# Kernel optimization log

Measured on AMD Instinct MI355X. Metric: run time of the kernel, lower is better.

The kernel has to match this reference:

```python
import jax, jax.numpy as jnp
import numpy as np

B, N_IN, N_OUT = 8192, 2048, 2048


def setup_inputs() -> dict:
    key = jax.random.key(0)
    kx, kw = jax.random.split(key)
    x = jax.random.normal(kx, (B, N_IN), dtype=jnp.float32)
    # torch: uniform_(-0.5, 0.5)
    weight = jax.random.uniform(kw, (N_IN, N_OUT), dtype=jnp.float32, minval=-0.5, maxval=0.5)
    return {"x": x, "weight": weight}


def reference(x, weight):
    # Binarize: W > 0 -> {0, 1}; then dense matmul (batch, n_in) @ (n_in, n_out)
    w_bin = (weight > 0).astype(x.dtype)
    return x @ w_bin
```

## Files before the change

kernel.cpp:

```cpp
#include <hip/hip_runtime.h>


#define MDIM 8192
#define NDIM 2048
#define KDIM 2048
#define NT   (KDIM / 128)
#define CH   (64 * KDIM)
#define BUFS 49152

typedef __attribute__((ext_vector_type(8))) short short8;
typedef __attribute__((ext_vector_type(4))) float float4v;
typedef __attribute__((ext_vector_type(4))) float f32x4;
typedef __attribute__((ext_vector_type(4))) int int4v;
typedef __attribute__((ext_vector_type(4))) unsigned short ushort4v;
typedef __attribute__((ext_vector_type(8))) unsigned short ushort8v;

__device__ __forceinline__ unsigned short f2bf(float f) {
    union { float f; unsigned u; } v; v.f = f;
    unsigned r = v.u + 0x7FFFu + ((v.u >> 16) & 1u);
    return (unsigned short)(r >> 16);
}

__device__ __forceinline__ void gload_lds16(void* l, const void* g) {
    __builtin_amdgcn_global_load_lds(
        (const __attribute__((address_space(1))) unsigned int*)g,
        (__attribute__((address_space(3))) unsigned int*)l,
        16, 0, 0);
}

#define FENCE asm volatile("" ::: "memory")
#define BAR do { FENCE; __builtin_amdgcn_s_barrier(); FENCE; } while (0)

__global__ __launch_bounds__(256) void prep(const float* __restrict__ X,
                                            const float* __restrict__ W,
                                            signed char* __restrict__ Xq,
                                            signed char* __restrict__ Wt,
                                            float* __restrict__ Sc) {
    __shared__ __align__(16) signed char T[64][80];
    __shared__ float wm[4];
    const int t = threadIdx.x;
    const int bid = blockIdx.x;

    if (bid < MDIM) {
        const int row = bid;
        const float* xr = X + (size_t)row * KDIM + t * 8;
        float4v a = *reinterpret_cast<const float4v*>(xr);
        float4v b = *reinterpret_cast<const float4v*>(xr + 4);
        float m = fabsf(a[0]);
        m = fmaxf(m, fabsf(a[1])); m = fmaxf(m, fabsf(a[2])); m = fmaxf(m, fabsf(a[3]));
        m = fmaxf(m, fabsf(b[0])); m = fmaxf(m, fabsf(b[1]));
        m = fmaxf(m, fabsf(b[2])); m = fmaxf(m, fabsf(b[3]));
#pragma unroll
        for (int off = 32; off; off >>= 1)
            m = fmaxf(m, __shfl_xor(m, off));
        if ((t & 63) == 0) wm[t >> 6] = m;
        __syncthreads();
        const float s = fmaxf(fmaxf(wm[0], wm[1]), fmaxf(wm[2], wm[3]));
        const float inv = (s > 0.f) ? 127.0f / s : 0.f;

        int q[8];
        q[0] = __float2int_rn(a[0] * inv); q[1] = __float2int_rn(a[1] * inv);
        q[2] = __float2int_rn(a[2] * inv); q[3] = __float2int_rn(a[3] * inv);
        q[4] = __float2int_rn(b[0] * inv); q[5] = __float2int_rn(b[1] * inv);
        q[6] = __float2int_rn(b[2] * inv); q[7] = __float2int_rn(b[3] * inv);
        unsigned lo = (q[0] & 255) | ((q[1] & 255) << 8) | ((q[2] & 255) << 16) | ((unsigned)(q[3] & 255) << 24);
        unsigned hi = (q[4] & 255) | ((q[5] & 255) << 8) | ((q[6] & 255) << 16) | ((unsigned)(q[7] & 255) << 24);
        unsigned* dst = (unsigned*)(Xq + (size_t)row * KDIM + t * 8);
        dst[0] = lo; dst[1] = hi;
        if (t == 0) Sc[row] = s * (1.0f / 127.0f);
    } else {
        const int wb = bid - MDIM;
        const int k0 = (wb >> 5) * 64;
        const int n0 = (wb & 31) * 64;
        const int kr = t >> 4;
        const int nc = (t & 15) * 4;
#pragma unroll
        for (int rr = 0; rr < 4; ++rr) {
            int k = k0 + rr * 16 + kr;
            float4v w4 = *reinterpret_cast<const float4v*>(W + (size_t)k * NDIM + n0 + nc);
#pragma unroll
            for (int c = 0; c < 4; ++c)
                T[nc + c][rr * 16 + kr] = (w4[c] > 0.0f) ? (signed char)1 : (signed char)0;
        }
        __syncthreads();
        const int row = t >> 2, ch = t & 3;
        int4v v = *reinterpret_cast<const int4v*>(&T[row][ch * 16]);
        *reinterpret_cast<int4v*>(Wt + (size_t)(n0 + row) * KDIM + k0 + ch * 16) = v;
    }
}

__global__ __launch_bounds__(512, 1) void gemm_2t(const signed char* __restrict__ A,
                                                  const signed char* __restrict__ Bt,
                                                  const float* __restrict__ Sc,
                                                  float* __restrict__ O) {
    extern __shared__ char lds[];
    const int tid  = threadIdx.x;
    const int lane = tid & 63;
    const int w    = tid >> 6;
    const int wr   = w >> 1;
    const int wc   = w & 1;

    int id  = blockIdx.x;
    int swz = (id & 7) * 32 + (id >> 3);
    const int bm  = swz >> 3;
    const int bnh = swz & 7;

    const int l3 = lane >> 3, l7 = lane & 7;
    const int srcOff = (w * 8 + l3) * KDIM + ((l7 ^ l3) << 4);
    const char* gA = (const char*)A + (size_t)(bm * 256) * KDIM + srcOff;

    const int fr = lane & 15, fg = lane >> 4;
    const int se0 = ((fg)     ^ (fr & 7)) << 4;
    const int se1 = ((4 + fg) ^ (fr & 7)) << 4;
    const int aRd = (wr * 64 + fr) * 128;
    const int bRd = 32768 + (wc * 64 + fr) * 128;

    {
        const char* gB0 = (const char*)Bt + (size_t)(bnh * 256) * KDIM + srcOff;
#pragma unroll
        for (int c = 0; c < 4; ++c)
            gload_lds16(lds + c * 8192 + w * 1024, gA + (size_t)c * CH);
#pragma unroll
        for (int c = 0; c < 2; ++c)
            gload_lds16(lds + 32768 + c * 8192 + w * 1024, gB0 + (size_t)c * CH);
    }

    for (int tt = 0; tt < 2; ++tt) {
        const char* gB  = (const char*)Bt + (size_t)(bnh * 256 + tt * 128) * KDIM + srcOff;
        const char* gB2 = (const char*)Bt + (size_t)(bnh * 256 + 128) * KDIM + srcOff;

        int4v acc[4][4];
#pragma unroll
        for (int i = 0; i < 4; ++i)
#pragma unroll
            for (int j = 0; j < 4; ++j) {
                acc[i][j][0] = 0; acc[i][j][1] = 0; acc[i][j][2] = 0; acc[i][j][3] = 0;
            }

        for (int t = 0; t < NT; ++t) {
            const int cur = (t & 1) * BUFS;
            const int nxt = ((t + 1) & 1) * BUFS;

            if (t == 0 && tt == 1) asm volatile("s_waitcnt vmcnt(63)" ::: "memory");
            else                   asm volatile("s_waitcnt vmcnt(0)" ::: "memory");
            BAR;

            if (t + 1 < NT) {
                const char* aN = gA + (size_t)(t + 1) * 128;
                const char* bN = gB + (size_t)(t + 1) * 128;
#pragma unroll
                for (int c = 0; c < 4; ++c)
                    gload_lds16(lds + nxt + c * 8192 + w * 1024, aN + (size_t)c * CH);
#pragma unroll
                for (int c = 0; c < 2; ++c)
                    gload_lds16(lds + nxt + 32768 + c * 8192 + w * 1024, bN + (size_t)c * CH);
            } else if (tt == 0) {
#pragma unroll
                for (int c = 0; c < 4; ++c)
                    gload_lds16(lds + nxt + c * 8192 + w * 1024, gA + (size_t)c * CH);
#pragma unroll
                for (int c = 0; c < 2; ++c)
                    gload_lds16(lds + nxt + 32768 + c * 8192 + w * 1024, gB2 + (size_t)c * CH);
            }

            int4v af[4], bf[4];
#pragma unroll
            for (int mi = 0; mi < 4; ++mi)
                af[mi] = *reinterpret_cast<const int4v*>(lds + cur + aRd + mi * 2048 + se0);
#pragma unroll
            for (int ni = 0; ni < 4; ++ni)
                bf[ni] = *reinterpret_cast<const int4v*>(lds + cur + bRd + ni * 2048 + se0);
            __builtin_amdgcn_s_setprio(1);
#pragma unroll
            for (int mi = 0; mi < 4; ++mi)
#pragma unroll
                for (int ni = 0; ni < 4; ++ni)
                    acc[mi][ni] = __builtin_amdgcn_mfma_i32_16x16x64_i8(
                        af[mi], bf[ni], acc[mi][ni], 0, 0, 0);
            __builtin_amdgcn_s_setprio(0);

#pragma unroll
            for (int mi = 0; mi < 4; ++mi)
                af[mi] = *reinterpret_cast<const int4v*>(lds + cur + aRd + mi * 2048 + se1);
#pragma unroll
            for (int ni = 0; ni < 4; ++ni)
                bf[ni] = *reinterpret_cast<const int4v*>(lds + cur + bRd + ni * 2048 + se1);
            __builtin_amdgcn_s_setprio(1);
#pragma unroll
            for (int mi = 0; mi < 4; ++mi)
#pragma unroll
                for (int ni = 0; ni < 4; ++ni)
                    acc[mi][ni] = __builtin_amdgcn_mfma_i32_16x16x64_i8(
                        af[mi], bf[ni], acc[mi][ni], 0, 0, 0);
            __builtin_amdgcn_s_setprio(0);
            FENCE;
        }

        const int orow0 = bm * 256 + wr * 64 + fg * 4;
        const int ocol0 = bnh * 256 + tt * 128 + wc * 64 + fr;
#pragma unroll
        for (int mi = 0; mi < 4; ++mi)
#pragma unroll
            for (int r = 0; r < 4; ++r) {
                const int row = orow0 + mi * 16 + r;
                const float s = Sc[row];
                float* op = O + (size_t)row * NDIM + ocol0;
#pragma unroll
                for (int ni = 0; ni < 4; ++ni)
                    op[ni * 16] = s * (float)acc[mi][ni][r];
            }
        FENCE;
    }
}

__global__ __launch_bounds__(256, 2) void binlin_fused(
        const float* __restrict__ X, const float* __restrict__ W,
        float* __restrict__ O) {
    const int tid = threadIdx.x;
    const int lane = tid & 63;
    const int wave = tid >> 6;
    const int wr = wave >> 1, wc = wave & 1;
    const int NWG = (MDIM / 128) * (NDIM / 128);
    int id = blockIdx.x;
    int swz = (id & 7) * (NWG >> 3) + (id >> 3);
    const int bm = swz >> 4, bn = swz & 15;

    __shared__ __align__(16) unsigned short As[128][40];
    __shared__ __align__(16) unsigned short Bs[128][40];

    const int rA = tid >> 3, kA = (tid & 7) * 4;
    const float* aPtr = X + (size_t)(bm * 128 + rA) * KDIM + kA;
    const int nB = (tid & 31) * 4, kB = (tid >> 5) * 4;
    const float* bPtr = W + (size_t)kB * NDIM + (size_t)bn * 128 + nB;

    float4v aReg[4], bReg[4];
#pragma unroll
    for (int p = 0; p < 4; ++p)
        aReg[p] = *reinterpret_cast<const float4v*>(aPtr + (size_t)(32 * p) * KDIM);
#pragma unroll
    for (int dk = 0; dk < 4; ++dk)
        bReg[dk] = *reinterpret_cast<const float4v*>(bPtr + (size_t)dk * NDIM);

    f32x4 acc[4][4];
#pragma unroll
    for (int i = 0; i < 4; ++i)
#pragma unroll
        for (int j = 0; j < 4; ++j) {
            acc[i][j][0] = 0.f; acc[i][j][1] = 0.f; acc[i][j][2] = 0.f; acc[i][j][3] = 0.f;
        }

    const int r16 = lane & 15, g8 = (lane >> 4) * 8;
    for (int kt = 0; kt < KDIM; kt += 32) {
#pragma unroll
        for (int p = 0; p < 4; ++p) {
            ushort4v v;
            v[0] = f2bf(aReg[p][0]); v[1] = f2bf(aReg[p][1]);
            v[2] = f2bf(aReg[p][2]); v[3] = f2bf(aReg[p][3]);
            *reinterpret_cast<ushort4v*>(&As[rA + 32 * p][kA]) = v;
        }
        unsigned short bb[4][4];
#pragma unroll
        for (int dk = 0; dk < 4; ++dk)
#pragma unroll
            for (int dn = 0; dn < 4; ++dn)
                bb[dn][dk] = (bReg[dk][dn] > 0.0f) ? (unsigned short)0x3F80u
                                                   : (unsigned short)0u;
#pragma unroll
        for (int dn = 0; dn < 4; ++dn) {
            ushort4v v;
            v[0] = bb[dn][0]; v[1] = bb[dn][1]; v[2] = bb[dn][2]; v[3] = bb[dn][3];
            *reinterpret_cast<ushort4v*>(&Bs[nB + dn][kB]) = v;
        }
        __syncthreads();
        if (kt + 32 < KDIM) {
#pragma unroll
            for (int p = 0; p < 4; ++p)
                aReg[p] = *reinterpret_cast<const float4v*>(
                    aPtr + (size_t)(32 * p) * KDIM + (kt + 32));
#pragma unroll
            for (int dk = 0; dk < 4; ++dk)
                bReg[dk] = *reinterpret_cast<const float4v*>(
                    bPtr + (size_t)(kt + 32 + dk) * NDIM);
        }
        short8 af[4], bfv[4];
#pragma unroll
        for (int mi = 0; mi < 4; ++mi)
            af[mi] = *reinterpret_cast<const short8*>(&As[wr * 64 + mi * 16 + r16][g8]);
#pragma unroll
        for (int ni = 0; ni < 4; ++ni)
            bfv[ni] = *reinterpret_cast<const short8*>(&Bs[wc * 64 + ni * 16 + r16][g8]);
#pragma unroll
        for (int mi = 0; mi < 4; ++mi)
#pragma unroll
            for (int ni = 0; ni < 4; ++ni)
                acc[mi][ni] = __builtin_amdgcn_mfma_f32_16x16x32_bf16(
                    af[mi], bfv[ni], acc[mi][ni], 0, 0, 0);
        __syncthreads();
    }

    const int orow0 = bm * 128 + wr * 64 + (lane >> 4) * 4;
    const int ocol0 = bn * 128 + wc * 64 + r16;
#pragma unroll
    for (int mi = 0; mi < 4; ++mi)
#pragma unroll
        for (int ni = 0; ni < 4; ++ni)
#pragma unroll
            for (int r = 0; r < 4; ++r)
                O[(size_t)(orow0 + mi * 16 + r) * NDIM + ocol0 + ni * 16] =
                    acc[mi][ni][r];
}

extern "C" void kernel_launch(void* const* d_in, const int* in_sizes, int n_in,
                              void* d_out, int out_size, void* d_ws, size_t ws_size,
                              hipStream_t stream) {
    const float* X = (const float*)d_in[0];
    const float* W = (const float*)d_in[1];
    float* O = (float*)d_out;
    (void)in_sizes; (void)n_in; (void)out_size;

    const size_t xq_bytes = (size_t)MDIM * KDIM;
    const size_t wt_bytes = (size_t)NDIM * KDIM;
    const size_t sc_bytes = (size_t)MDIM * sizeof(float);
    const size_t need = xq_bytes + wt_bytes + sc_bytes;

    if (ws_size >= need) {
        signed char* Xq = (signed char*)d_ws;
        signed char* Wt = Xq + xq_bytes;
        float* Sc = (float*)(Wt + wt_bytes);
        hipFuncSetAttribute((const void*)gemm_2t,
                            hipFuncAttributeMaxDynamicSharedMemorySize, 98304);
        prep<<<dim3(MDIM + (KDIM / 64) * (NDIM / 64)), dim3(256), 0, stream>>>(X, W, Xq, Wt, Sc);
        gemm_2t<<<dim3((MDIM / 256) * (NDIM / 256)), dim3(512), 98304, stream>>>(Xq, Wt, Sc, O);
    } else {
        binlin_fused<<<dim3((MDIM / 128) * (NDIM / 128)), dim3(256), 0, stream>>>(X, W, O);
    }
}
```

Measured before the change: 59.21 us.

## Switch int8 GEMM to triple-buffered LDS pipeline with 256x128 tiles

Replaces the double-buffered GEMM, where each workgroup computed two 128-column halves one after the other, with a triple-buffered pipeline that prefetches two k-steps ahead and waits with vmcnt(6) instead of draining all loads. Each workgroup now computes a single 256x128 tile, so the grid doubles to 512 workgroups and the swizzle changes to match. The goal is to hide global-to-LDS latency better and raise CU utilisation. The cost is 144KB of LDS per workgroup, and the A tile is no longer reused across two N halves, so A traffic goes up.

```diff
diff --git a/kernel.cpp b/kernel.cpp
--- a/kernel.cpp
+++ b/kernel.cpp
@@ -6,7 +6,7 @@
 #define KDIM 2048
 #define NT   (KDIM / 128)
 #define CH   (64 * KDIM)
-#define BUFS 49152
+#define BUF  49152
 
 typedef __attribute__((ext_vector_type(8))) short short8;
 typedef __attribute__((ext_vector_type(4))) float float4v;
@@ -89,10 +89,10 @@
     }
 }
 
-__global__ __launch_bounds__(512, 1) void gemm_2t(const signed char* __restrict__ A,
-                                                  const signed char* __restrict__ Bt,
-                                                  const float* __restrict__ Sc,
-                                                  float* __restrict__ O) {
+__global__ __launch_bounds__(512, 1) void gemm_tri(const signed char* __restrict__ A,
+                                                   const signed char* __restrict__ Bt,
+                                                   const float* __restrict__ Sc,
+                                                   float* __restrict__ O) {
     extern __shared__ char lds[];
     const int tid  = threadIdx.x;
     const int lane = tid & 63;
@@ -101,13 +101,14 @@
     const int wc   = w & 1;
 
     int id  = blockIdx.x;
-    int swz = (id & 7) * 32 + (id >> 3);
-    const int bm  = swz >> 3;
-    const int bnh = swz & 7;
+    int swz = (id & 7) * 64 + (id >> 3);
+    const int bm = swz >> 4;
+    const int bn = swz & 15;
 
     const int l3 = lane >> 3, l7 = lane & 7;
     const int srcOff = (w * 8 + l3) * KDIM + ((l7 ^ l3) << 4);
     const char* gA = (const char*)A + (size_t)(bm * 256) * KDIM + srcOff;
+    const char* gB = (const char*)Bt + (size_t)(bn * 128) * KDIM + srcOff;
 
     const int fr = lane & 15, fg = lane >> 4;
     const int se0 = ((fg)     ^ (fr & 7)) << 4;
@@ -115,102 +116,98 @@
     const int aRd = (wr * 64 + fr) * 128;
     const int bRd = 32768 + (wc * 64 + fr) * 128;
 
-    {
-        const char* gB0 = (const char*)Bt + (size_t)(bnh * 256) * KDIM + srcOff;
-#pragma unroll
-        for (int c = 0; c < 4; ++c)
-            gload_lds16(lds + c * 8192 + w * 1024, gA + (size_t)c * CH);
-#pragma unroll
-        for (int c = 0; c < 2; ++c)
-            gload_lds16(lds + 32768 + c * 8192 + w * 1024, gB0 + (size_t)c * CH);
+    int4v acc[4][4];
+#pragma unroll
+    for (int i = 0; i < 4; ++i)
+#pragma unroll
+        for (int j = 0; j < 4; ++j) {
+            acc[i][j][0] = 0; acc[i][j][1] = 0; acc[i][j][2] = 0; acc[i][j][3] = 0;
+        }
+
+#pragma unroll
+    for (int c = 0; c < 4; ++c)
+        gload_lds16(lds + c * 8192 + w * 1024, gA + (size_t)c * CH);
+#pragma unroll
+    for (int c = 0; c < 2; ++c)
+        gload_lds16(lds + 32768 + c * 8192 + w * 1024, gB + (size_t)c * CH);
+#pragma unroll
+    for (int c = 0; c < 4; ++c)
+        gload_lds16(lds + BUF + c * 8192 + w * 1024, gA + 128 + (size_t)c * CH);
+#pragma unroll
+    for (int c = 0; c < 2; ++c)
+        gload_lds16(lds + BUF + 32768 + c * 8192 + w * 1024, gB + 128 + (size_t)c * CH);
+
+    int b3 = 0;
+    int s3 = 2;
+    for (int t = 0; t < NT; ++t) {
+        const int cur = b3 * BUF;
+        const bool moreS = (t + 2 < NT);
+
+        if (t == NT - 1) asm volatile("s_waitcnt vmcnt(0)" ::: "memory");
+        else             asm volatile("s_waitcnt vmcnt(6)" ::: "memory");
+        BAR;
+
+        if (moreS) {
+            const int st = s3 * BUF;
+            const char* aN = gA + (size_t)(t + 2) * 128;
+            const char* bN = gB + (size_t)(t + 2) * 128;
+#pragma unroll
+            for (int c = 0; c < 4; ++c)
+                gload_lds16(lds + st + c * 8192 + w * 1024, aN + (size_t)c * CH);
+#pragma unroll
+            for (int c = 0; c < 2; ++c)
+                gload_lds16(lds + st + 32768 + c * 8192 + w * 1024, bN + (size_t)c * CH);
+        }
+
+        int4v af[4], bf[4];
+#pragma unroll
+        for (int mi = 0; mi < 4; ++mi)
+            af[mi] = *reinterpret_cast<const int4v*>(lds + cur + aRd + mi * 2048 + se0);
+#pragma unroll
+        for (int ni = 0; ni < 4; ++ni)
+            bf[ni] = *reinterpret_cast<const int4v*>(lds + cur + bRd + ni * 2048 + se0);
+        __builtin_amdgcn_s_setprio(1);
+#pragma unroll
+        for (int mi = 0; mi < 4; ++mi)
+#pragma unroll
+            for (int ni = 0; ni < 4; ++ni)
+                acc[mi][ni] = __builtin_amdgcn_mfma_i32_16x16x64_i8(
+                    af[mi], bf[ni], acc[mi][ni], 0, 0, 0);
+        __builtin_amdgcn_s_setprio(0);
+
+#pragma unroll
+        for (int mi = 0; mi < 4; ++mi)
+            af[mi] = *reinterpret_cast<const int4v*>(lds + cur + aRd + mi * 2048 + se1);
+#pragma unroll
+        for (int ni = 0; ni < 4; ++ni)
+            bf[ni] = *reinterpret_cast<const int4v*>(lds + cur + bRd + ni * 2048 + se1);
+        __builtin_amdgcn_s_setprio(1);
+#pragma unroll
+        for (int mi = 0; mi < 4; ++mi)
+#pragma unroll
+            for (int ni = 0; ni < 4; ++ni)
+                acc[mi][ni] = __builtin_amdgcn_mfma_i32_16x16x64_i8(
+                    af[mi], bf[ni], acc[mi][ni], 0, 0, 0);
+        __builtin_amdgcn_s_setprio(0);
+        FENCE;
+
+        b3 = (b3 == 2) ? 0 : b3 + 1;
+        s3 = (s3 == 2) ? 0 : s3 + 1;
     }
 
-    for (int tt = 0; tt < 2; ++tt) {
-        const char* gB  = (const char*)Bt + (size_t)(bnh * 256 + tt * 128) * KDIM + srcOff;
-        const char* gB2 = (const char*)Bt + (size_t)(bnh * 256 + 128) * KDIM + srcOff;
-
-        int4v acc[4][4];
-#pragma unroll
-        for (int i = 0; i < 4; ++i)
-#pragma unroll
-            for (int j = 0; j < 4; ++j) {
-                acc[i][j][0] = 0; acc[i][j][1] = 0; acc[i][j][2] = 0; acc[i][j][3] = 0;
-            }
-
-        for (int t = 0; t < NT; ++t) {
-            const int cur = (t & 1) * BUFS;
-            const int nxt = ((t + 1) & 1) * BUFS;
-
-            if (t == 0 && tt == 1) asm volatile("s_waitcnt vmcnt(63)" ::: "memory");
-            else                   asm volatile("s_waitcnt vmcnt(0)" ::: "memory");
-            BAR;
-
-            if (t + 1 < NT) {
-                const char* aN = gA + (size_t)(t + 1) * 128;
-                const char* bN = gB + (size_t)(t + 1) * 128;
-#pragma unroll
-                for (int c = 0; c < 4; ++c)
-                    gload_lds16(lds + nxt + c * 8192 + w * 1024, aN + (size_t)c * CH);
-#pragma unroll
-                for (int c = 0; c < 2; ++c)
-                    gload_lds16(lds + nxt + 32768 + c * 8192 + w * 1024, bN + (size_t)c * CH);
-            } else if (tt == 0) {
-#pragma unroll
-                for (int c = 0; c < 4; ++c)
-                    gload_lds16(lds + nxt + c * 8192 + w * 1024, gA + (size_t)c * CH);
-#pragma unroll
-                for (int c = 0; c < 2; ++c)
-                    gload_lds16(lds + nxt + 32768 + c * 8192 + w * 1024, gB2 + (size_t)c * CH);
-            }
-
-            int4v af[4], bf[4];
-#pragma unroll
-            for (int mi = 0; mi < 4; ++mi)
-                af[mi] = *reinterpret_cast<const int4v*>(lds + cur + aRd + mi * 2048 + se0);
+    const int orow0 = bm * 256 + wr * 64 + fg * 4;
+    const int ocol0 = bn * 128 + wc * 64 + fr;
+#pragma unroll
+    for (int mi = 0; mi < 4; ++mi)
+#pragma unroll
+        for (int r = 0; r < 4; ++r) {
+            const int row = orow0 + mi * 16 + r;
+            const float s = Sc[row];
+            float* op = O + (size_t)row * NDIM + ocol0;
 #pragma unroll
             for (int ni = 0; ni < 4; ++ni)
-                bf[ni] = *reinterpret_cast<const int4v*>(lds + cur + bRd + ni * 2048 + se0);
-            __builtin_amdgcn_s_setprio(1);
-#pragma unroll
-            for (int mi = 0; mi < 4; ++mi)
-#pragma unroll
-                for (int ni = 0; ni < 4; ++ni)
-                    acc[mi][ni] = __builtin_amdgcn_mfma_i32_16x16x64_i8(
-                        af[mi], bf[ni], acc[mi][ni], 0, 0, 0);
-            __builtin_amdgcn_s_setprio(0);
-
-#pragma unroll
-            for (int mi = 0; mi < 4; ++mi)
-                af[mi] = *reinterpret_cast<const int4v*>(lds + cur + aRd + mi * 2048 + se1);
-#pragma unroll
-            for (int ni = 0; ni < 4; ++ni)
-                bf[ni] = *reinterpret_cast<const int4v*>(lds + cur + bRd + ni * 2048 + se1);
-            __builtin_amdgcn_s_setprio(1);
-#pragma unroll
-            for (int mi = 0; mi < 4; ++mi)
-#pragma unroll
-                for (int ni = 0; ni < 4; ++ni)
-                    acc[mi][ni] = __builtin_amdgcn_mfma_i32_16x16x64_i8(
-                        af[mi], bf[ni], acc[mi][ni], 0, 0, 0);
-            __builtin_amdgcn_s_setprio(0);
-            FENCE;
-        }
-
-        const int orow0 = bm * 256 + wr * 64 + fg * 4;
-        const int ocol0 = bnh * 256 + tt * 128 + wc * 64 + fr;
-#pragma unroll
-        for (int mi = 0; mi < 4; ++mi)
-#pragma unroll
-            for (int r = 0; r < 4; ++r) {
-                const int row = orow0 + mi * 16 + r;
-                const float s = Sc[row];
-                float* op = O + (size_t)row * NDIM + ocol0;
-#pragma unroll
-                for (int ni = 0; ni < 4; ++ni)
-                    op[ni * 16] = s * (float)acc[mi][ni][r];
-            }
-        FENCE;
-    }
+                op[ni * 16] = s * (float)acc[mi][ni][r];
+        }
 }
 
 __global__ __launch_bounds__(256, 2) void binlin_fused(
@@ -327,10 +324,10 @@
         signed char* Xq = (signed char*)d_ws;
         signed char* Wt = Xq + xq_bytes;
         float* Sc = (float*)(Wt + wt_bytes);
-        hipFuncSetAttribute((const void*)gemm_2t,
-                            hipFuncAttributeMaxDynamicSharedMemorySize, 98304);
+        hipFuncSetAttribute((const void*)gemm_tri,
+                            hipFuncAttributeMaxDynamicSharedMemorySize, 3 * BUF);
         prep<<<dim3(MDIM + (KDIM / 64) * (NDIM / 64)), dim3(256), 0, stream>>>(X, W, Xq, Wt, Sc);
-        gemm_2t<<<dim3((MDIM / 256) * (NDIM / 256)), dim3(512), 98304, stream>>>(Xq, Wt, Sc, O);
+        gemm_tri<<<dim3((MDIM / 256) * (NDIM / 128)), dim3(512), 3 * BUF, stream>>>(Xq, Wt, Sc, O);
     } else {
         binlin_fused<<<dim3((MDIM / 128) * (NDIM / 128)), dim3(256), 0, stream>>>(X, W, O);
     }
```

New measurement: 61.22 us. 3.4% more time.
